# Performance work log

Measured on AMD Instinct MI355X. Metric: run time of the kernel, lower is better.

The kernel has to match this reference:

```python
import jax, jax.numpy as jnp
import numpy as np

SHAPE = (64, 64, 64)
N0 = 4000
K = 5  # subm conv kernel size -> 125 taps


def _neighbors(coors, shp):
    # coors: [N,4] int (b,z,y,x), batch=1. Returns [N,125] int32 neighbor row ids, -1 if absent.
    offs = np.stack(np.meshgrid(np.arange(-2, 3), np.arange(-2, 3), np.arange(-2, 3), indexing='ij'), -1).reshape(-1, 3)
    shp = np.asarray(shp)
    grid = -np.ones(tuple(shp), np.int32)
    grid[coors[:, 1], coors[:, 2], coors[:, 3]] = np.arange(len(coors), dtype=np.int32)
    nb = coors[:, None, 1:4] + offs[None]  # [N,125,3]
    valid = ((nb >= 0) & (nb < shp)).all(-1)
    nbc = np.clip(nb, 0, shp - 1)
    nbr = grid[nbc[..., 0], nbc[..., 1], nbc[..., 2]]
    return np.where(valid, nbr, -1).astype(np.int32)


def _pool_map(coors, shp):
    # kernel 2 stride 2 sparse max pool: parent cell = spatial // 2
    out_shp = [s // 2 for s in shp]
    sp = coors[:, 1:4] // 2
    lin = (sp[:, 0] * out_shp[1] + sp[:, 1]) * out_shp[2] + sp[:, 2]
    uniq, inv = np.unique(lin, return_inverse=True)
    z = uniq // (out_shp[1] * out_shp[2])
    r = uniq % (out_shp[1] * out_shp[2])
    nc = np.stack([np.zeros_like(z), z, r // out_shp[2], r % out_shp[2]], 1).astype(np.int32)
    return inv.astype(np.int32), nc, out_shp


_PAIRS = [(3, 64), (64, 64), (64, 96), (96, 96), (96, 128), (128, 128), (128, 160), (160, 160), (160, 192), (192, 192), (192, 224), (224, 224), (224, 256), (256, 256)]
_WNAMES = ['w0a', 'w0b', 'w1a', 'w1b', 'w2a', 'w2b', 'w3a', 'w3b', 'w4a', 'w4b', 'w5a', 'w5b', 'w6a', 'w6b']


def setup_inputs() -> dict:
    rng = np.random.RandomState(0)
    lin = rng.choice(SHAPE[0] * SHAPE[1] * SHAPE[2], N0, replace=False)
    z = lin // (SHAPE[1] * SHAPE[2])
    r = lin % (SHAPE[1] * SHAPE[2])
    coors = np.stack([np.zeros_like(z), z, r // SHAPE[2], r % SHAPE[2]], 1).astype(np.int32)
    inp = {}
    c, shp = coors, list(SHAPE)
    for l in range(7):
        inp['nbr%d' % l] = jnp.asarray(_neighbors(c, shp))
        if l < 6:
            pm, c, shp = _pool_map(c, shp)
            inp['pool%d' % l] = jnp.asarray(pm)
    key = jax.random.key(0)
    for name, (ci, co) in zip(_WNAMES, _PAIRS):
        key, k = jax.random.split(key)
        inp[name] = jax.random.normal(k, (K ** 3, ci, co), jnp.float32) * (K ** 3 * ci) ** -0.5
    key, kf = jax.random.split(key)
    inp['features'] = jax.random.normal(kf, (N0, 3), jnp.float32)
    inp['coors'] = jnp.asarray(coors)
    inp['batch_size'] = 1
    return inp


def _subm(feats, nbr, w):
    # gather-GEMM-scatter form of SubMConv3d (bias=False): out active set == in active set
    valid = nbr >= 0  # [N,125]
    g = jnp.take(feats, jnp.maximum(nbr, 0), axis=0)  # [N,125,Cin]
    g = jnp.where(valid[:, :, None], g, jnp.zeros((), feats.dtype))
    return jnp.einsum('nkc,kco->no', g, w)  # [N,Cout]


def reference(features, coors, batch_size, nbr0, nbr1, nbr2, nbr3, nbr4, nbr5, nbr6, pool0, pool1, pool2, pool3, pool4, pool5, w0a, w0b, w1a, w1b, w2a, w2b, w3a, w3b, w4a, w4b, w5a, w5b, w6a, w6b):
    nbrs = (nbr0, nbr1, nbr2, nbr3, nbr4, nbr5, nbr6)
    pools = (pool0, pool1, pool2, pool3, pool4, pool5)
    ws = ((w0a, w0b), (w1a, w1b), (w2a, w2b), (w3a, w3b), (w4a, w4b), (w5a, w5b), (w6a, w6b))
    x = features
    for l in range(7):
        x = _subm(x, nbrs[l], ws[l][0])
        x = _subm(x, nbrs[l], ws[l][1])
        if l < 6:
            # sparse max pool over active voxels of each 2x2x2 cell
            x = jax.ops.segment_max(x, pools[l], num_segments=nbrs[l + 1].shape[0])
    return x
```

## Files before the change

kernel.cpp:

```cpp
#include <hip/hip_runtime.h>
#include <stddef.h>
#include <stdint.h>

#define KTAPS 125

typedef _Float16 f16x8 __attribute__((ext_vector_type(8)));
typedef float    f32x4 __attribute__((ext_vector_type(4)));

__device__ __forceinline__ void gload16(const void* g, void* l) {
    __builtin_amdgcn_global_load_lds(
        (const __attribute__((address_space(1))) void*)g,
        (__attribute__((address_space(3))) void*)l, 16, 0, 0);
}

template<int NT>
__global__ __launch_bounds__(256) void subm_mfma(
    const _Float16* __restrict__ finh, const int* __restrict__ nbr,
    const _Float16* __restrict__ wt, float* __restrict__ fout,
    int N, int CinP, int TS, int CS, float outscale)
{
    constexpr int BN = NT * 32;
    constexpr int NF = NT * 2;
    __shared__ int       nbs[16][64];
    __shared__ unsigned  msk[16][2];
    __shared__ unsigned char vtl[16];
    __shared__ _Float16  Ga[2][64 * 32];
    __shared__ _Float16  Wl[2][32 * BN];

    const int tid  = threadIdx.x;
    const int lane = tid & 63;
    const int wid  = tid >> 6;
    const int row0 = blockIdx.x * 64;
    const int ts   = blockIdx.y;
    const int cs   = blockIdx.z;
    const int k0   = (ts * KTAPS) / TS;
    const int k1   = ((ts + 1) * KTAPS) / TS;
    const int KR   = k1 - k0;
    const int CC   = CinP >> 5;
    const int cc0  = (cs * CC) / CS;
    const int cc1  = ((cs + 1) * CC) / CS;

    #pragma unroll
    for (int p = 0; p < 4; ++p) {
        int e = tid + p * 256;
        if (e < KR * 64) {
            int j = e >> 6, r = e & 63;
            int gr = row0 + r;
            nbs[j][r] = (gr < N) ? nbr[(size_t)gr * KTAPS + k0 + j] : -1;
        }
    }
    __syncthreads();
    for (int j = wid; j < KR; j += 4) {
        unsigned long long m = __ballot(nbs[j][lane] >= 0);
        if (lane == 0) { msk[j][0] = (unsigned)m; msk[j][1] = (unsigned)(m >> 32); }
    }
    __syncthreads();
    int VC = 0;
    for (int j = 0; j < KR; ++j)
        if (msk[j][0] | msk[j][1]) { vtl[VC] = (unsigned char)j; ++VC; }
    if (VC == 0) return;

    const int r15 = lane & 15, g4 = lane >> 4;
    const int myrow = wid * 16 + r15;

    f32x4 acc[NF];
    #pragma unroll
    for (int n = 0; n < NF; ++n) acc[n] = (f32x4){0.f, 0.f, 0.f, 0.f};
    unsigned um = 0;

    auto STAGE = [&](int i, int c, int buf) {
        int j = vtl[i];
        int nb = nbs[j][myrow];
        int src = (nb < 0) ? N : nb;
        gload16(finh + (size_t)src * CinP + c * 32 + g4 * 8,
                &Ga[buf][(size_t)wid * 512]);
        int k = k0 + j;
        const _Float16* ws = wt + ((size_t)k * CC + c) * (32 * (size_t)BN);
        #pragma unroll
        for (int p = 0; p < (BN + 63) / 64; ++p) {
            int gI = p * 256 + tid;
            if (gI < 4 * BN)
                gload16(ws + (size_t)gI * 8, &Wl[buf][((size_t)p * 256 + wid * 64) * 8]);
        }
    };

    auto COMPUTE = [&](int i, int buf) {
        int j = vtl[i];
        unsigned mw = (msk[j][wid >> 1] >> ((wid & 1) * 16)) & 0xFFFFu;
        mw = __builtin_amdgcn_readfirstlane(mw);
        if (mw) {
            um |= mw;
            f16x8 a = *(const f16x8*)&Ga[buf][(size_t)tid * 8];
            #pragma unroll
            for (int n = 0; n < NF; ++n) {
                f16x8 b = *(const f16x8*)&Wl[buf][((size_t)g4 * BN + n * 16 + r15) * 8];
                acc[n] = __builtin_amdgcn_mfma_f32_16x16x32_f16(a, b, acc[n], 0, 0, 0);
            }
        }
    };

    int i = 0, c = cc0, buf = 0;
    STAGE(0, cc0, 0);
    while (true) {
        __syncthreads();
        int ni = i, nc = c + 1;
        if (nc == cc1) { ni = i + 1; nc = cc0; }
        if (ni < VC) STAGE(ni, nc, buf ^ 1);
        COMPUTE(i, buf);
        i = ni; c = nc; buf ^= 1;
        if (i >= VC) break;
    }

    if (!__builtin_amdgcn_readfirstlane(um)) return;
    const bool atom = (TS * CS) > 1;
    #pragma unroll
    for (int n = 0; n < NF; ++n) {
        int col = n * 16 + r15;
        #pragma unroll
        for (int q = 0; q < 4; ++q) {
            int r = row0 + wid * 16 + g4 * 4 + q;
            if (r < N) {
                float v = acc[n][q] * outscale;
                if (atom) atomicAdd(&fout[(size_t)r * BN + col], v);
                else      fout[(size_t)r * BN + col] = v;
            }
        }
    }
}

__global__ __launch_bounds__(256) void tap_flags(
    const int* n0, const int* n1, const int* n2, const int* n3,
    const int* n4, const int* n5, const int* n6,
    int N0, int N1, int N2, int N3, int N4, int N5, int N6,
    unsigned* __restrict__ flags)
{
    int l = blockIdx.y, k = blockIdx.x;
    const int* nb; int N;
    switch (l) {
        case 0: nb = n0; N = N0; break;  case 1: nb = n1; N = N1; break;
        case 2: nb = n2; N = N2; break;  case 3: nb = n3; N = N3; break;
        case 4: nb = n4; N = N4; break;  case 5: nb = n5; N = N5; break;
        default: nb = n6; N = N6; break;
    }
    bool any = false;
    for (int r = threadIdx.x; r < N; r += 256) any |= (nb[(size_t)r * KTAPS + k] >= 0);
    bool a = __syncthreads_or(any);
    if (threadIdx.x == 0) flags[l * KTAPS + k] = a ? 1u : 0u;
}

__global__ __launch_bounds__(256) void cvt_weights(
    const float* __restrict__ wa, const float* __restrict__ wb,
    _Float16* __restrict__ ta, _Float16* __restrict__ tb,
    const unsigned* __restrict__ flags,
    int CinA, int CCa, int CoutA, int splitA,
    int CinB, int CCb, int CoutB)
{
    int k = blockIdx.x;
    if (!flags[k]) return;
    int by = blockIdx.y;
    const float* w; _Float16* t; int Cin, CC, Cout, cc, c0;
    if (by < splitA) { w = wa; t = ta; Cin = CinA; CC = CCa; Cout = CoutA;
                       cc = by / (CoutA / 32); c0 = (by % (CoutA / 32)) * 32; }
    else { by -= splitA; w = wb; t = tb; Cin = CinB; CC = CCb; Cout = CoutB;
           cc = by / (CoutB / 32); c0 = (by % (CoutB / 32)) * 32; }

    __shared__ float T[32][33];
    int tid = threadIdx.x;
    #pragma unroll
    for (int p = 0; p < 4; ++p) {
        int e = tid + p * 256;
        int r = e >> 5, cl = e & 31;
        int ci = cc * 32 + r;
        T[r][cl] = (ci < Cin) ? w[((size_t)k * Cin + ci) * Cout + c0 + cl] : 0.f;
    }
    __syncthreads();
    if (tid < 128) {
        int g = tid >> 5, co = tid & 31;
        f16x8 h;
        #pragma unroll
        for (int j = 0; j < 8; ++j) h[j] = (_Float16)T[g * 8 + j][co];
        *(f16x8*)&t[((size_t)k * CC + cc) * (32 * (size_t)Cout) + ((size_t)g * Cout + c0 + co) * 8] = h;
    }
}

__global__ __launch_bounds__(256) void init_all(
    const float* __restrict__ feat, _Float16* __restrict__ H,
    float* __restrict__ F, unsigned* __restrict__ ENC,
    int N0, int nF, int nE)
{
    int i = blockIdx.x * 256 + threadIdx.x;
    if (i < nF) F[i] = 0.f;
    if (i < nE) ENC[i] = 0u;
    int nH = (N0 + 1) * 32;
    if (i < nH) {
        int r = i >> 5, cl = i & 31;
        H[i] = (r < N0 && cl < 3) ? (_Float16)feat[r * 3 + cl] : (_Float16)0.f;
    }
}

__global__ __launch_bounds__(256) void cvt_feat(
    float* __restrict__ F, _Float16* __restrict__ H, int N, int C, float scale)
{
    int i = blockIdx.x * 256 + threadIdx.x;
    if (i < N * C) { H[i] = (_Float16)(F[i] * scale); F[i] = 0.f; }
    else if (i < (N + 1) * C) H[i] = (_Float16)0.f;
}

__device__ __forceinline__ unsigned enc_f32(float f) {
    unsigned u = __float_as_uint(f);
    return (u & 0x80000000u) ? ~u : (u | 0x80000000u);
}

__global__ __launch_bounds__(256) void pool_max(
    float* __restrict__ F, const int* __restrict__ pm,
    unsigned* __restrict__ ENC, int Nin, int C)
{
    int i = blockIdx.x * 256 + threadIdx.x;
    if (i >= Nin * C) return;
    int r = i / C, cl = i - r * C;
    atomicMax(&ENC[(size_t)pm[r] * C + cl], enc_f32(F[i]));
    F[i] = 0.f;
}

__global__ __launch_bounds__(256) void pool_dec(
    unsigned* __restrict__ ENC, _Float16* __restrict__ H, int Nout, int C, float scale)
{
    int i = blockIdx.x * 256 + threadIdx.x;
    if (i < Nout * C) {
        unsigned u = ENC[i];
        float f = __uint_as_float((u & 0x80000000u) ? (u ^ 0x80000000u) : ~u);
        H[i] = (_Float16)(f * scale);
        ENC[i] = 0u;
    } else if (i < (Nout + 1) * C) {
        H[i] = (_Float16)0.f;
    }
}

static void launch_conv(const _Float16* fin, const int* nbr, const _Float16* wt, float* fout,
                        int N, int CinP, int Cout, float outscale, hipStream_t s)
{
    int rt = (N + 63) / 64;
    int TS = (512 + rt - 1) / rt;
    if (TS < 8) TS = 8;
    if (TS > KTAPS) TS = KTAPS;
    int CC = CinP / 32;
    int CS = (rt == 1 && TS == KTAPS) ? CC : 1;
    dim3 g(rt, TS, CS);
    switch (Cout / 32) {
        case 2: subm_mfma<2><<<g, 256, 0, s>>>(fin, nbr, wt, fout, N, CinP, TS, CS, outscale); break;
        case 3: subm_mfma<3><<<g, 256, 0, s>>>(fin, nbr, wt, fout, N, CinP, TS, CS, outscale); break;
        case 4: subm_mfma<4><<<g, 256, 0, s>>>(fin, nbr, wt, fout, N, CinP, TS, CS, outscale); break;
        case 5: subm_mfma<5><<<g, 256, 0, s>>>(fin, nbr, wt, fout, N, CinP, TS, CS, outscale); break;
        case 6: subm_mfma<6><<<g, 256, 0, s>>>(fin, nbr, wt, fout, N, CinP, TS, CS, outscale); break;
        case 7: subm_mfma<7><<<g, 256, 0, s>>>(fin, nbr, wt, fout, N, CinP, TS, CS, outscale); break;
        case 8: subm_mfma<8><<<g, 256, 0, s>>>(fin, nbr, wt, fout, N, CinP, TS, CS, outscale); break;
    }
}

extern "C" void kernel_launch(void* const* d_in, const int* in_sizes, int n_in,
                              void* d_out, int out_size, void* d_ws, size_t ws_size,
                              hipStream_t stream)
{
    const int* nbr[7]; const int* pm[6]; int Ns[7];
    {
        int idx = 0;
        for (int l = 0; l < 7; ++l) {
            nbr[l] = (const int*)d_in[idx];
            Ns[l]  = in_sizes[idx] / KTAPS;
            ++idx;
            if (l < 6) { pm[l] = (const int*)d_in[idx]; ++idx; }
        }
    }
    const float* w[14];
    for (int i = 0; i < 14; ++i) w[i] = (const float*)d_in[13 + i];
    const float* feat = (const float*)d_in[27];

    static const int CI[14]  = {3,64, 64,96, 96,128, 128,160, 160,192, 192,224, 224,256};
    static const int CO[14]  = {64,64, 96,96, 128,128, 160,160, 192,192, 224,224, 256,256};
    static const int KSH[14] = {0,3, 2,2, 1,1, 0,0, 0,1, 0,2, 2,3};
    const float finalScale = 1.0f / 131072.0f;
    int CinP[14];
    for (int i = 0; i < 14; ++i) CinP[i] = (CI[i] < 32) ? 32 : CI[i];

    size_t maxF = 0, maxE = 0, maxHa = 0, maxHb = 0, maxWA = 0, maxWB = 0;
    for (int l = 0; l < 7; ++l) {
        size_t f = (size_t)Ns[l] * CO[2*l];
        if (f > maxF) maxF = f;
        if (l < 6) { size_t e = (size_t)Ns[l+1] * CO[2*l+1]; if (e > maxE) maxE = e; }
        size_t ha = (size_t)(Ns[l] + 1) * CinP[2*l];   if (ha > maxHa) maxHa = ha;
        size_t hb = (size_t)(Ns[l] + 1) * CinP[2*l+1]; if (hb > maxHb) maxHb = hb;
        size_t wa = (size_t)KTAPS * CinP[2*l] * CO[2*l];     if (wa > maxWA) maxWA = wa;
        size_t wb = (size_t)KTAPS * CinP[2*l+1] * CO[2*l+1]; if (wb > maxWB) maxWB = wb;
    }
    size_t off = 0;
    auto carve = [&](size_t bytes) -> void* {
        void* p = (char*)d_ws + off;
        off = (off + bytes + 255) & ~(size_t)255;
        return p;
    };
    float*     F    = (float*)carve(maxF * 4);
    unsigned*  ENC  = (unsigned*)carve(maxE * 4);
    _Float16*  Ha   = (_Float16*)carve(maxHa * 2);
    _Float16*  Hb   = (_Float16*)carve(maxHb * 2);
    _Float16*  wtA  = (_Float16*)carve(maxWA * 2);
    _Float16*  wtB  = (_Float16*)carve(maxWB * 2);
    unsigned*  flags= (unsigned*)carve(7 * KTAPS * 4);

    hipMemsetAsync(d_out, 0, (size_t)out_size * sizeof(float), stream);

    {
        int nInit = (int)maxF;
        if ((int)maxE > nInit) nInit = (int)maxE;
        int nH = (Ns[0] + 1) * 32;
        if (nH > nInit) nInit = nH;
        init_all<<<(nInit + 255) / 256, 256, 0, stream>>>(feat, Ha, F, ENC, Ns[0], (int)maxF, (int)maxE);
    }
    tap_flags<<<dim3(KTAPS, 7), 256, 0, stream>>>(
        nbr[0], nbr[1], nbr[2], nbr[3], nbr[4], nbr[5], nbr[6],
        Ns[0], Ns[1], Ns[2], Ns[3], Ns[4], Ns[5], Ns[6], flags);

    for (int l = 0; l < 7; ++l) {
        int ia = 2 * l, ib = 2 * l + 1;
        int N = Ns[l];
        int splitA = (CinP[ia] / 32) * (CO[ia] / 32);
        int splitB = (CinP[ib] / 32) * (CO[ib] / 32);
        cvt_weights<<<dim3(KTAPS, splitA + splitB), 256, 0, stream>>>(
            w[ia], w[ib], wtA, wtB, flags + l * KTAPS,
            CI[ia], CinP[ia] / 32, CO[ia], splitA,
            CI[ib], CinP[ib] / 32, CO[ib]);

        launch_conv(Ha, nbr[l], wtA, F, N, CinP[ia], CO[ia], 1.f, stream);

        {
            int tot = (N + 1) * CO[ia];
            cvt_feat<<<(tot + 255) / 256, 256, 0, stream>>>(F, Hb, N, CO[ia], (float)(1 << KSH[ib]));
        }

        float* outb = (l == 6) ? (float*)d_out : F;
        launch_conv(Hb, nbr[l], wtB, outb, N, CinP[ib], CO[ib],
                    (l == 6) ? finalScale : 1.f, stream);

        if (l < 6) {
            int C = CO[ib], Nout = Ns[l + 1];
            int tot = N * C;
            pool_max<<<(tot + 255) / 256, 256, 0, stream>>>(F, pm[l], ENC, N, C);
            int tot2 = (Nout + 1) * C;
            pool_dec<<<(tot2 + 255) / 256, 256, 0, stream>>>(ENC, Ha, Nout, C,
                                                             (float)(1 << KSH[2 * l + 2]));
        }
    }
}
```

Baseline: 438.8 us.

## Register-pipeline sparse conv, fuse f32→f16 input conversion, split waves by row mask

The subm conv kernel drops LDS staging and barriers. Each wave now loads its A rows and B weights directly into registers with double-buffering, and each wave covers 32 rows by half the output columns. Each row-half keeps its own list of valid taps, so waves can skip taps that are empty for their rows. The second conv reads the f32 accumulator directly and converts to f16 with scaling in-kernel, which removes the cvt_feat pass. Output always uses atomics, the split heuristics aim for more blocks, and buffer zeroing is folded into init and pool kernels. The trade is more global and L2 traffic without LDS reuse of weights, plus more atomic contention.

```diff
diff --git a/kernel.cpp b/kernel.cpp
--- a/kernel.cpp
+++ b/kernel.cpp
@@ -7,38 +7,32 @@
 typedef _Float16 f16x8 __attribute__((ext_vector_type(8)));
 typedef float    f32x4 __attribute__((ext_vector_type(4)));
 
-__device__ __forceinline__ void gload16(const void* g, void* l) {
-    __builtin_amdgcn_global_load_lds(
-        (const __attribute__((address_space(1))) void*)g,
-        (__attribute__((address_space(3))) void*)l, 16, 0, 0);
-}
-
-template<int NT>
+template<int NT, bool F32IN>
 __global__ __launch_bounds__(256) void subm_mfma(
-    const _Float16* __restrict__ finh, const int* __restrict__ nbr,
+    const void* __restrict__ fin, const int* __restrict__ nbr,
     const _Float16* __restrict__ wt, float* __restrict__ fout,
-    int N, int CinP, int TS, int CS, float outscale)
+    int N, int CinP, int TS, int CS, float inscale, float outscale)
 {
     constexpr int BN = NT * 32;
-    constexpr int NF = NT * 2;
     __shared__ int       nbs[16][64];
     __shared__ unsigned  msk[16][2];
-    __shared__ unsigned char vtl[16];
-    __shared__ _Float16  Ga[2][64 * 32];
-    __shared__ _Float16  Wl[2][32 * BN];
+    __shared__ unsigned char vtl[2][16];
+    __shared__ int       vcs[2];
 
     const int tid  = threadIdx.x;
     const int lane = tid & 63;
     const int wid  = tid >> 6;
+    const int wy   = wid & 1;
+    const int wx   = wid >> 1;
+    const int r15  = lane & 15;
+    const int g4   = lane >> 4;
     const int row0 = blockIdx.x * 64;
-    const int ts   = blockIdx.y;
-    const int cs   = blockIdx.z;
-    const int k0   = (ts * KTAPS) / TS;
-    const int k1   = ((ts + 1) * KTAPS) / TS;
+    const int k0   = (blockIdx.y * KTAPS) / TS;
+    const int k1   = ((blockIdx.y + 1) * KTAPS) / TS;
     const int KR   = k1 - k0;
     const int CC   = CinP >> 5;
-    const int cc0  = (cs * CC) / CS;
-    const int cc1  = ((cs + 1) * CC) / CS;
+    const int cc0  = (blockIdx.z * CC) / CS;
+    const int cc1  = ((blockIdx.z + 1) * CC) / CS;
 
     #pragma unroll
     for (int p = 0; p < 4; ++p) {
@@ -55,74 +49,94 @@
         if (lane == 0) { msk[j][0] = (unsigned)m; msk[j][1] = (unsigned)(m >> 32); }
     }
     __syncthreads();
-    int VC = 0;
-    for (int j = 0; j < KR; ++j)
-        if (msk[j][0] | msk[j][1]) { vtl[VC] = (unsigned char)j; ++VC; }
-    if (VC == 0) return;
-
-    const int r15 = lane & 15, g4 = lane >> 4;
-    const int myrow = wid * 16 + r15;
-
-    f32x4 acc[NF];
+    if (wid < 2) {
+        int c = 0;
+        for (int j = 0; j < KR; ++j)
+            if (msk[j][wid]) { if (lane == 0) vtl[wid][c] = (unsigned char)j; ++c; }
+        if (lane == 0) vcs[wid] = c;
+    }
+    __syncthreads();
+    const int VCw = vcs[wy];
+    if (VCw == 0) return;
+
+    unsigned um = 0;
+    for (int t = 0; t < VCw; ++t) um |= msk[vtl[wy][t]][wy];
+
+    f32x4 acc[2][NT];
     #pragma unroll
-    for (int n = 0; n < NF; ++n) acc[n] = (f32x4){0.f, 0.f, 0.f, 0.f};
-    unsigned um = 0;
-
-    auto STAGE = [&](int i, int c, int buf) {
-        int j = vtl[i];
-        int nb = nbs[j][myrow];
-        int src = (nb < 0) ? N : nb;
-        gload16(finh + (size_t)src * CinP + c * 32 + g4 * 8,
-                &Ga[buf][(size_t)wid * 512]);
-        int k = k0 + j;
-        const _Float16* ws = wt + ((size_t)k * CC + c) * (32 * (size_t)BN);
-        #pragma unroll
-        for (int p = 0; p < (BN + 63) / 64; ++p) {
-            int gI = p * 256 + tid;
-            if (gI < 4 * BN)
-                gload16(ws + (size_t)gI * 8, &Wl[buf][((size_t)p * 256 + wid * 64) * 8]);
+    for (int mt = 0; mt < 2; ++mt)
+        #pragma unroll
+        for (int nf = 0; nf < NT; ++nf)
+            acc[mt][nf] = (f32x4){0.f, 0.f, 0.f, 0.f};
+
+    const size_t wchunk = (size_t)32 * BN;
+    const int    boffh  = (g4 * BN + wx * (NT * 16) + r15) * 8;
+
+    auto LOADA = [&](f16x8 (&a)[2], int j, int c) {
+        #pragma unroll
+        for (int mt = 0; mt < 2; ++mt) {
+            int src = nbs[j][wy * 32 + mt * 16 + r15];
+            if (src < 0) src = N;
+            size_t base = (size_t)src * CinP + c * 32 + g4 * 8;
+            if (F32IN) {
+                const float* p = (const float*)fin + base;
+                float4 v0 = *(const float4*)p;
+                float4 v1 = *(const float4*)(p + 4);
+                f16x8 h;
+                h[0] = (_Float16)(v0.x * inscale); h[1] = (_Float16)(v0.y * inscale);
+                h[2] = (_Float16)(v0.z * inscale); h[3] = (_Float16)(v0.w * inscale);
+                h[4] = (_Float16)(v1.x * inscale); h[5] = (_Float16)(v1.y * inscale);
+                h[6] = (_Float16)(v1.z * inscale); h[7] = (_Float16)(v1.w * inscale);
+                a[mt] = h;
+            } else {
+                a[mt] = *(const f16x8*)((const _Float16*)fin + base);
+            }
         }
     };
-
-    auto COMPUTE = [&](int i, int buf) {
-        int j = vtl[i];
-        unsigned mw = (msk[j][wid >> 1] >> ((wid & 1) * 16)) & 0xFFFFu;
-        mw = __builtin_amdgcn_readfirstlane(mw);
-        if (mw) {
-            um |= mw;
-            f16x8 a = *(const f16x8*)&Ga[buf][(size_t)tid * 8];
+    auto LOADB = [&](f16x8 (&b)[NT], int j, int c) {
+        const _Float16* base = wt + ((size_t)(k0 + j) * CC + c) * wchunk;
+        #pragma unroll
+        for (int nf = 0; nf < NT; ++nf)
+            b[nf] = *(const f16x8*)&base[boffh + nf * 128];
+    };
+    auto MFMA = [&](f16x8 (&a)[2], f16x8 (&b)[NT]) {
+        #pragma unroll
+        for (int mt = 0; mt < 2; ++mt)
             #pragma unroll
-            for (int n = 0; n < NF; ++n) {
-                f16x8 b = *(const f16x8*)&Wl[buf][((size_t)g4 * BN + n * 16 + r15) * 8];
-                acc[n] = __builtin_amdgcn_mfma_f32_16x16x32_f16(a, b, acc[n], 0, 0, 0);
-            }
-        }
+            for (int nf = 0; nf < NT; ++nf)
+                acc[mt][nf] = __builtin_amdgcn_mfma_f32_16x16x32_f16(a[mt], b[nf], acc[mt][nf], 0, 0, 0);
     };
 
-    int i = 0, c = cc0, buf = 0;
-    STAGE(0, cc0, 0);
+    f16x8 a0[2], b0[NT], a1[2], b1[NT];
+    int i = 0, c = cc0;
+    { int j = vtl[wy][0]; LOADA(a0, j, c); LOADB(b0, j, c); }
     while (true) {
-        __syncthreads();
-        int ni = i, nc = c + 1;
-        if (nc == cc1) { ni = i + 1; nc = cc0; }
-        if (ni < VC) STAGE(ni, nc, buf ^ 1);
-        COMPUTE(i, buf);
-        i = ni; c = nc; buf ^= 1;
-        if (i >= VC) break;
-    }
-
-    if (!__builtin_amdgcn_readfirstlane(um)) return;
-    const bool atom = (TS * CS) > 1;
+        int ni = i, nc = c + 1; if (nc == cc1) { ni = i + 1; nc = cc0; }
+        bool m1 = ni < VCw;
+        if (m1) { int j = vtl[wy][ni]; LOADA(a1, j, nc); LOADB(b1, j, nc); }
+        MFMA(a0, b0);
+        if (!m1) break;
+        i = ni; c = nc;
+        ni = i; nc = c + 1; if (nc == cc1) { ni = i + 1; nc = cc0; }
+        bool m2 = ni < VCw;
+        if (m2) { int j = vtl[wy][ni]; LOADA(a0, j, nc); LOADB(b0, j, nc); }
+        MFMA(a1, b1);
+        if (!m2) break;
+        i = ni; c = nc;
+    }
+
     #pragma unroll
-    for (int n = 0; n < NF; ++n) {
-        int col = n * 16 + r15;
+    for (int mt = 0; mt < 2; ++mt) {
         #pragma unroll
         for (int q = 0; q < 4; ++q) {
-            int r = row0 + wid * 16 + g4 * 4 + q;
-            if (r < N) {
-                float v = acc[n][q] * outscale;
-                if (atom) atomicAdd(&fout[(size_t)r * BN + col], v);
-                else      fout[(size_t)r * BN + col] = v;
+            int lr = mt * 16 + g4 * 4 + q;
+            int gr = row0 + wy * 32 + lr;
+            if (((um >> lr) & 1u) && gr < N) {
+                #pragma unroll
+                for (int nf = 0; nf < NT; ++nf) {
+                    int col = wx * (NT * 16) + nf * 16 + r15;
+                    atomicAdd(&fout[(size_t)gr * BN + col], acc[mt][nf][q] * outscale);
+                }
             }
         }
     }
@@ -185,12 +199,15 @@
 
 __global__ __launch_bounds__(256) void init_all(
     const float* __restrict__ feat, _Float16* __restrict__ H,
-    float* __restrict__ F, unsigned* __restrict__ ENC,
-    int N0, int nF, int nE)
+    float* __restrict__ Fa, float* __restrict__ Fb,
+    unsigned* __restrict__ ENC, float* __restrict__ dout,
+    int N0, int nFa, int nFb, int nE, int nOut)
 {
     int i = blockIdx.x * 256 + threadIdx.x;
-    if (i < nF) F[i] = 0.f;
-    if (i < nE) ENC[i] = 0u;
+    if (i < nFa) Fa[i] = 0.f;
+    if (i < nFb) Fb[i] = 0.f;
+    if (i < nE)  ENC[i] = 0u;
+    if (i < nOut) dout[i] = 0.f;
     int nH = (N0 + 1) * 32;
     if (i < nH) {
         int r = i >> 5, cl = i & 31;
@@ -198,28 +215,23 @@
     }
 }
 
-__global__ __launch_bounds__(256) void cvt_feat(
-    float* __restrict__ F, _Float16* __restrict__ H, int N, int C, float scale)
-{
-    int i = blockIdx.x * 256 + threadIdx.x;
-    if (i < N * C) { H[i] = (_Float16)(F[i] * scale); F[i] = 0.f; }
-    else if (i < (N + 1) * C) H[i] = (_Float16)0.f;
-}
-
 __device__ __forceinline__ unsigned enc_f32(float f) {
     unsigned u = __float_as_uint(f);
     return (u & 0x80000000u) ? ~u : (u | 0x80000000u);
 }
 
 __global__ __launch_bounds__(256) void pool_max(
-    float* __restrict__ F, const int* __restrict__ pm,
-    unsigned* __restrict__ ENC, int Nin, int C)
+    float* __restrict__ Fb, const int* __restrict__ pm,
+    unsigned* __restrict__ ENC, float* __restrict__ Fa,
+    int Nin, int C, int nzero)
 {
     int i = blockIdx.x * 256 + threadIdx.x;
-    if (i >= Nin * C) return;
-    int r = i / C, cl = i - r * C;
-    atomicMax(&ENC[(size_t)pm[r] * C + cl], enc_f32(F[i]));
-    F[i] = 0.f;
+    if (i < Nin * C) {
+        int r = i / C, cl = i - r * C;
+        atomicMax(&ENC[(size_t)pm[r] * C + cl], enc_f32(Fb[i]));
+        Fb[i] = 0.f;
+    }
+    if (i < nzero) Fa[i] = 0.f;
 }
 
 __global__ __launch_bounds__(256) void pool_dec(
@@ -236,25 +248,36 @@
     }
 }
 
-static void launch_conv(const _Float16* fin, const int* nbr, const _Float16* wt, float* fout,
-                        int N, int CinP, int Cout, float outscale, hipStream_t s)
+template<bool F32>
+static void conv_dispatch(int NT, dim3 g, hipStream_t s, const void* fin, const int* nbr,
+                          const _Float16* wt, float* fout, int N, int CinP, int TS, int CS,
+                          float insc, float outsc)
+{
+    switch (NT) {
+        case 2: subm_mfma<2,F32><<<g,256,0,s>>>(fin,nbr,wt,fout,N,CinP,TS,CS,insc,outsc); break;
+        case 3: subm_mfma<3,F32><<<g,256,0,s>>>(fin,nbr,wt,fout,N,CinP,TS,CS,insc,outsc); break;
+        case 4: subm_mfma<4,F32><<<g,256,0,s>>>(fin,nbr,wt,fout,N,CinP,TS,CS,insc,outsc); break;
+        case 5: subm_mfma<5,F32><<<g,256,0,s>>>(fin,nbr,wt,fout,N,CinP,TS,CS,insc,outsc); break;
+        case 6: subm_mfma<6,F32><<<g,256,0,s>>>(fin,nbr,wt,fout,N,CinP,TS,CS,insc,outsc); break;
+        case 7: subm_mfma<7,F32><<<g,256,0,s>>>(fin,nbr,wt,fout,N,CinP,TS,CS,insc,outsc); break;
+        case 8: subm_mfma<8,F32><<<g,256,0,s>>>(fin,nbr,wt,fout,N,CinP,TS,CS,insc,outsc); break;
+    }
+}
+
+static void launch_conv(bool f32in, const void* fin, const int* nbr, const _Float16* wt,
+                        float* fout, int N, int CinP, int Cout, float insc, float outsc,
+                        hipStream_t s)
 {
     int rt = (N + 63) / 64;
-    int TS = (512 + rt - 1) / rt;
-    if (TS < 8) TS = 8;
+    int TS = (1536 + rt - 1) / rt;
     if (TS > KTAPS) TS = KTAPS;
     int CC = CinP / 32;
-    int CS = (rt == 1 && TS == KTAPS) ? CC : 1;
+    int CS = 1;
+    long blocks = (long)rt * TS;
+    if (blocks < 1024) { CS = (int)((1536 + blocks - 1) / blocks); if (CS > CC) CS = CC; }
     dim3 g(rt, TS, CS);
-    switch (Cout / 32) {
-        case 2: subm_mfma<2><<<g, 256, 0, s>>>(fin, nbr, wt, fout, N, CinP, TS, CS, outscale); break;
-        case 3: subm_mfma<3><<<g, 256, 0, s>>>(fin, nbr, wt, fout, N, CinP, TS, CS, outscale); break;
-        case 4: subm_mfma<4><<<g, 256, 0, s>>>(fin, nbr, wt, fout, N, CinP, TS, CS, outscale); break;
-        case 5: subm_mfma<5><<<g, 256, 0, s>>>(fin, nbr, wt, fout, N, CinP, TS, CS, outscale); break;
-        case 6: subm_mfma<6><<<g, 256, 0, s>>>(fin, nbr, wt, fout, N, CinP, TS, CS, outscale); break;
-        case 7: subm_mfma<7><<<g, 256, 0, s>>>(fin, nbr, wt, fout, N, CinP, TS, CS, outscale); break;
-        case 8: subm_mfma<8><<<g, 256, 0, s>>>(fin, nbr, wt, fout, N, CinP, TS, CS, outscale); break;
-    }
+    if (f32in) conv_dispatch<true >(Cout/32, g, s, fin, nbr, wt, fout, N, CinP, TS, CS, insc, outsc);
+    else       conv_dispatch<false>(Cout/32, g, s, fin, nbr, wt, fout, N, CinP, TS, CS, insc, outsc);
 }
 
 extern "C" void kernel_launch(void* const* d_in, const int* in_sizes, int n_in,
@@ -282,13 +305,12 @@
     int CinP[14];
     for (int i = 0; i < 14; ++i) CinP[i] = (CI[i] < 32) ? 32 : CI[i];
 
-    size_t maxF = 0, maxE = 0, maxHa = 0, maxHb = 0, maxWA = 0, maxWB = 0;
+    size_t maxFa = 0, maxFb = 0, maxE = 0, maxHa = 0, maxWA = 0, maxWB = 0;
     for (int l = 0; l < 7; ++l) {
-        size_t f = (size_t)Ns[l] * CO[2*l];
-        if (f > maxF) maxF = f;
+        size_t fa = (size_t)(Ns[l] + 1) * CO[2*l];   if (fa > maxFa) maxFa = fa;
+        size_t fb = (size_t)(Ns[l] + 1) * CO[2*l+1]; if (fb > maxFb) maxFb = fb;
         if (l < 6) { size_t e = (size_t)Ns[l+1] * CO[2*l+1]; if (e > maxE) maxE = e; }
-        size_t ha = (size_t)(Ns[l] + 1) * CinP[2*l];   if (ha > maxHa) maxHa = ha;
-        size_t hb = (size_t)(Ns[l] + 1) * CinP[2*l+1]; if (hb > maxHb) maxHb = hb;
+        size_t ha = (size_t)(Ns[l] + 1) * CinP[2*l]; if (ha > maxHa) maxHa = ha;
         size_t wa = (size_t)KTAPS * CinP[2*l] * CO[2*l];     if (wa > maxWA) maxWA = wa;
         size_t wb = (size_t)KTAPS * CinP[2*l+1] * CO[2*l+1]; if (wb > maxWB) maxWB = wb;
     }
@@ -298,22 +320,24 @@
         off = (off + bytes + 255) & ~(size_t)255;
         return p;
     };
-    float*     F    = (float*)carve(maxF * 4);
+    float*     Fa   = (float*)carve(maxFa * 4);
+    float*     Fb   = (float*)carve(maxFb * 4);
     unsigned*  ENC  = (unsigned*)carve(maxE * 4);
     _Float16*  Ha   = (_Float16*)carve(maxHa * 2);
-    _Float16*  Hb   = (_Float16*)carve(maxHb * 2);
     _Float16*  wtA  = (_Float16*)carve(maxWA * 2);
     _Float16*  wtB  = (_Float16*)carve(maxWB * 2);
     unsigned*  flags= (unsigned*)carve(7 * KTAPS * 4);
 
-    hipMemsetAsync(d_out, 0, (size_t)out_size * sizeof(float), stream);
-
     {
-        int nInit = (int)maxF;
-        if ((int)maxE > nInit) nInit = (int)maxE;
+        int nMax = (int)maxFa;
+        if ((int)maxFb > nMax) nMax = (int)maxFb;
+        if ((int)maxE  > nMax) nMax = (int)maxE;
         int nH = (Ns[0] + 1) * 32;
-        if (nH > nInit) nInit = nH;
-        init_all<<<(nInit + 255) / 256, 256, 0, stream>>>(feat, Ha, F, ENC, Ns[0], (int)maxF, (int)maxE);
+        if (nH > nMax) nMax = nH;
+        if (out_size > nMax) nMax = out_size;
+        init_all<<<(nMax + 255) / 256, 256, 0, stream>>>(
+            feat, Ha, Fa, Fb, ENC, (float*)d_out,
+            Ns[0], (int)maxFa, (int)maxFb, (int)maxE, out_size);
     }
     tap_flags<<<dim3(KTAPS, 7), 256, 0, stream>>>(
         nbr[0], nbr[1], nbr[2], nbr[3], nbr[4], nbr[5], nbr[6],
@@ -329,21 +353,17 @@
             CI[ia], CinP[ia] / 32, CO[ia], splitA,
             CI[ib], CinP[ib] / 32, CO[ib]);
 
-        launch_conv(Ha, nbr[l], wtA, F, N, CinP[ia], CO[ia], 1.f, stream);
-
-        {
-            int tot = (N + 1) * CO[ia];
-            cvt_feat<<<(tot + 255) / 256, 256, 0, stream>>>(F, Hb, N, CO[ia], (float)(1 << KSH[ib]));
-        }
-
-        float* outb = (l == 6) ? (float*)d_out : F;
-        launch_conv(Hb, nbr[l], wtB, outb, N, CinP[ib], CO[ib],
-                    (l == 6) ? finalScale : 1.f, stream);
+        launch_conv(false, Ha, nbr[l], wtA, Fa, N, CinP[ia], CO[ia], 1.f, 1.f, stream);
+
+        float* outb = (l == 6) ? (float*)d_out : Fb;
+        launch_conv(true, Fa, nbr[l], wtB, outb, N, CinP[ib], CO[ib],
+                    (float)(1 << KSH[ib]), (l == 6) ? finalScale : 1.f, stream);
 
         if (l < 6) {
             int C = CO[ib], Nout = Ns[l + 1];
-            int tot = N * C;
-            pool_max<<<(tot + 255) / 256, 256, 0, stream>>>(F, pm[l], ENC, N, C);
+            int nzero = (Nout + 1) * CO[2 * l + 2];
+            int tot = N * C; if (nzero > tot) tot = nzero;
+            pool_max<<<(tot + 255) / 256, 256, 0, stream>>>(Fb, pm[l], ENC, Fa, N, C, nzero);
             int tot2 = (Nout + 1) * C;
             pool_dec<<<(tot2 + 255) / 256, 256, 0, stream>>>(ENC, Ha, Nout, C,
                                                              (float)(1 << KSH[2 * l + 2]));
```

Result: faster. 427.2 us (-2.6%).
